# Performance work log

Hardware: AMD Instinct MI355X
Metric: run time of the kernel (lower is better)

Reference implementation:

```python
import jax, jax.numpy as jnp
from jax import lax
import numpy as np

BS, L, D, K, R, VOCAB = 4096, 200, 64, 4, 3, 100000
DROP = jnp.float32(-(1 << 31))


def squash(caps):
    # caps: (bs, K, D)
    n = jnp.linalg.norm(caps, axis=2, keepdims=True)   # (bs, K, 1)
    n2 = n * n
    return n2 / ((1.0 + n2) * n + 1e-9) * caps


def setup_inputs() -> dict:
    key = jax.random.key(0)
    ks = jax.random.split(key, 8)
    his = jax.random.randint(ks[0], (BS, L), 0, VOCAB)                     # item ids, 0 = pad
    E = jax.random.normal(ks[1], (VOCAB, D), dtype=jnp.float32)            # itemEmbeds.weight
    S = jax.random.normal(ks[2], (D, D), dtype=jnp.float32)                # bilinear map S
    B0 = jax.random.normal(ks[3], (K, L), dtype=jnp.float32)               # routing logits
    lim1 = 1.0 / np.sqrt(D)
    W1 = jax.random.uniform(ks[4], (D, 4 * D), jnp.float32, -lim1, lim1)   # dense1 (in, out)
    b1 = jax.random.uniform(ks[5], (4 * D,), jnp.float32, -lim1, lim1)
    lim2 = 1.0 / np.sqrt(4 * D)
    W2 = jax.random.uniform(ks[6], (4 * D, D), jnp.float32, -lim2, lim2)   # dense2 (in, out)
    b2 = jax.random.uniform(ks[7], (D,), jnp.float32, -lim2, lim2)
    return {"his": his, "E": E, "S": S, "B0": B0, "W1": W1, "b1": b1, "W2": W2, "b2": b2}


def reference(his, E, S, B0, W1, b1, W2, b2):
    bs = his.shape[0]
    # padding_idx=0 -> embedding row 0 is zero
    E = E.at[0].set(0.0)
    mask = (his != 0)[:, None, :]                       # (bs, 1, L), broadcasts over K
    hisP = jnp.einsum('bld,de->ble', E[his], S)         # (bs, L, D)
    hisPd = lax.stop_gradient(hisP)                     # routing updates run under no_grad
    B = jnp.broadcast_to(lax.stop_gradient(B0)[None], (bs, K, L))
    for _ in range(R - 1):
        W = jax.nn.softmax(jnp.where(mask, B, DROP), axis=2)   # (bs, K, L)
        caps = squash(jnp.einsum('bkl,bld->bkd', W, hisPd))
        B = B + jnp.einsum('bkd,bld->bkl', caps, hisPd)
    W = jax.nn.softmax(jnp.where(mask, B, DROP), axis=2)
    caps = squash(jnp.einsum('bkl,bld->bkd', W, hisP))         # differentiable last iter
    h = jax.nn.relu(jnp.einsum('bkd,df->bkf', caps, W1) + b1)
    return jnp.einsum('bkf,fd->bkd', h, W2) + b2               # (bs, K, D)
```

## Files before the change

kernel.cpp:

```cpp
#include <hip/hip_runtime.h>

#define LSEQ 200
#define KCAP 4
#define NVOC 100000

__global__ __launch_bounds__(256) void precompute_P(
    const float* __restrict__ E, const float* __restrict__ S,
    float* __restrict__ P)
{
    __shared__ __align__(16) float Sl[64 * 64];
    __shared__ __align__(16) float Et[64 * 68];
    const int tid   = threadIdx.x;
    const int vbase = blockIdx.x * 64;

    #pragma unroll
    for (int t = tid; t < 4096; t += 256) Sl[t] = S[t];
    #pragma unroll
    for (int t = tid; t < 4096; t += 256) {
        int r = t >> 6, e = t & 63;
        int v = vbase + r;
        Et[e * 68 + r] = (v < NVOC) ? E[v * 64 + e] : 0.f;
    }
    __syncthreads();

    const int rq = tid >> 4;
    const int cq = tid & 15;
    float a00=0,a01=0,a02=0,a03=0, a10=0,a11=0,a12=0,a13=0;
    float a20=0,a21=0,a22=0,a23=0, a30=0,a31=0,a32=0,a33=0;
    #pragma unroll 8
    for (int e = 0; e < 64; e++) {
        float4 ev = *(const float4*)(Et + e * 68 + rq * 4);
        float4 sv = *(const float4*)(Sl + e * 64 + cq * 4);
        a00 = fmaf(ev.x, sv.x, a00); a01 = fmaf(ev.x, sv.y, a01);
        a02 = fmaf(ev.x, sv.z, a02); a03 = fmaf(ev.x, sv.w, a03);
        a10 = fmaf(ev.y, sv.x, a10); a11 = fmaf(ev.y, sv.y, a11);
        a12 = fmaf(ev.y, sv.z, a12); a13 = fmaf(ev.y, sv.w, a13);
        a20 = fmaf(ev.z, sv.x, a20); a21 = fmaf(ev.z, sv.y, a21);
        a22 = fmaf(ev.z, sv.z, a22); a23 = fmaf(ev.z, sv.w, a23);
        a30 = fmaf(ev.w, sv.x, a30); a31 = fmaf(ev.w, sv.y, a31);
        a32 = fmaf(ev.w, sv.z, a32); a33 = fmaf(ev.w, sv.w, a33);
    }

    const int r0 = vbase + rq * 4;
    float4 o0 = make_float4(a00, a01, a02, a03);
    float4 o1 = make_float4(a10, a11, a12, a13);
    float4 o2 = make_float4(a20, a21, a22, a23);
    float4 o3 = make_float4(a30, a31, a32, a33);
    if (r0 == 0) o0 = make_float4(0.f, 0.f, 0.f, 0.f);
    if (r0 + 0 < NVOC) *(float4*)(P + (r0 + 0) * 64 + cq * 4) = o0;
    if (r0 + 1 < NVOC) *(float4*)(P + (r0 + 1) * 64 + cq * 4) = o1;
    if (r0 + 2 < NVOC) *(float4*)(P + (r0 + 2) * 64 + cq * 4) = o2;
    if (r0 + 3 < NVOC) *(float4*)(P + (r0 + 3) * 64 + cq * 4) = o3;
}

__global__ __launch_bounds__(256)
__attribute__((amdgpu_waves_per_eu(4, 8)))
void mind_row(
    const int*   __restrict__ his, const float* __restrict__ P,
    const float* __restrict__ B0,  const float* __restrict__ W1,
    const float* __restrict__ b1,  const float* __restrict__ W2,
    const float* __restrict__ b2,  float* __restrict__ out)
{
    __shared__ __align__(16) float POOL[4336];
    float* Bm     = POOL;
    float* W4     = POOL + 832;
    float* caps4  = POOL + 1632;
    float* bigneg = POOL + 1888;
    int*   idxs   = (int*)(POOL + 2088);
    float* SC     = POOL + 2288;
    float* part   = SC;
    float* h4     = SC + 1024;

    const int b    = blockIdx.x;
    const int tid  = threadIdx.x;
    const int lane = tid & 63;
    const int wv   = tid >> 6;

    for (int l = tid; l < LSEQ; l += 256) {
        int id = his[b * LSEQ + l];
        idxs[l]   = id;
        bigneg[l] = (id != 0) ? 0.f : -1e30f;
    }
    if (tid < LSEQ) {
        #pragma unroll
        for (int k = 0; k < KCAP; k++) Bm[k * 208 + tid] = B0[k * LSEQ + tid];
    }
    __syncthreads();

    float hp[50];
    #pragma unroll
    for (int i = 0; i < 50; i++) {
        int l = wv * 50 + i;
        hp[i] = P[idxs[l] * 64 + lane];
    }

    for (int r = 0; r < 3; r++) {
        {
            const float* Bk = Bm + wv * 208;
            float x0 = Bk[lane]       + bigneg[lane];
            float x1 = Bk[lane + 64]  + bigneg[lane + 64];
            float x2 = Bk[lane + 128] + bigneg[lane + 128];
            float x3 = (lane < 8) ? (Bk[lane + 192] + bigneg[lane + 192]) : -3.0e38f;
            float m = fmaxf(fmaxf(x0, x1), fmaxf(x2, x3));
            #pragma unroll
            for (int off = 32; off; off >>= 1) m = fmaxf(m, __shfl_xor(m, off, 64));
            float e0 = __expf(x0 - m), e1 = __expf(x1 - m), e2 = __expf(x2 - m);
            float e3 = (lane < 8) ? __expf(x3 - m) : 0.f;
            float ssum = e0 + e1 + e2 + e3;
            #pragma unroll
            for (int off = 32; off; off >>= 1) ssum += __shfl_xor(ssum, off, 64);
            float inv = 1.f / ssum;
            W4[lane * 4 + wv]         = e0 * inv;
            W4[(lane + 64) * 4 + wv]  = e1 * inv;
            W4[(lane + 128) * 4 + wv] = e2 * inv;
            if (lane < 8) W4[(lane + 192) * 4 + wv] = e3 * inv;
        }
        __syncthreads();

        {
            float a0 = 0, a1 = 0, a2 = 0, a3 = 0;
            #pragma unroll
            for (int i = 0; i < 50; i++) {
                int l = wv * 50 + i;
                float4 w = *(const float4*)(W4 + l * 4);
                float  v = hp[i];
                a0 = fmaf(w.x, v, a0);
                a1 = fmaf(w.y, v, a1);
                a2 = fmaf(w.z, v, a2);
                a3 = fmaf(w.w, v, a3);
            }
            part[wv * 256 + lane]       = a0;
            part[wv * 256 + 64 + lane]  = a1;
            part[wv * 256 + 128 + lane] = a2;
            part[wv * 256 + 192 + lane] = a3;
        }
        __syncthreads();

        {
            float c = part[wv * 64 + lane]       + part[256 + wv * 64 + lane]
                    + part[512 + wv * 64 + lane] + part[768 + wv * 64 + lane];
            float n2 = c * c;
            #pragma unroll
            for (int off = 32; off; off >>= 1) n2 += __shfl_xor(n2, off, 64);
            float n  = sqrtf(n2);
            float sc = n2 / ((1.f + n2) * n + 1e-9f);
            c *= sc;
            caps4[lane * 4 + wv] = c;
        }
        __syncthreads();

        if (r < 2) {
            if (tid < LSEQ) {
                const float4* __restrict__ rowp = (const float4*)(P + idxs[tid] * 64);
                float d0 = 0, d1 = 0, d2 = 0, d3 = 0;
                #pragma unroll
                for (int j = 0; j < 16; j++) {
                    float4 v = rowp[j];
                    {
                        float4 c = *(const float4*)(caps4 + (j * 4 + 0) * 4);
                        d0 = fmaf(c.x, v.x, d0); d1 = fmaf(c.y, v.x, d1);
                        d2 = fmaf(c.z, v.x, d2); d3 = fmaf(c.w, v.x, d3);
                    }
                    {
                        float4 c = *(const float4*)(caps4 + (j * 4 + 1) * 4);
                        d0 = fmaf(c.x, v.y, d0); d1 = fmaf(c.y, v.y, d1);
                        d2 = fmaf(c.z, v.y, d2); d3 = fmaf(c.w, v.y, d3);
                    }
                    {
                        float4 c = *(const float4*)(caps4 + (j * 4 + 2) * 4);
                        d0 = fmaf(c.x, v.z, d0); d1 = fmaf(c.y, v.z, d1);
                        d2 = fmaf(c.z, v.z, d2); d3 = fmaf(c.w, v.z, d3);
                    }
                    {
                        float4 c = *(const float4*)(caps4 + (j * 4 + 3) * 4);
                        d0 = fmaf(c.x, v.w, d0); d1 = fmaf(c.y, v.w, d1);
                        d2 = fmaf(c.z, v.w, d2); d3 = fmaf(c.w, v.w, d3);
                    }
                }
                Bm[tid]       += d0;
                Bm[208 + tid] += d1;
                Bm[416 + tid] += d2;
                Bm[624 + tid] += d3;
            }
            __syncthreads();
        }
    }

    {
        const int f = tid;
        float h0 = 0, h1 = 0, h2 = 0, h3 = 0;
        #pragma unroll 8
        for (int d = 0; d < 64; d++) {
            float  w = W1[d * 256 + f];
            float4 c = *(const float4*)(caps4 + d * 4);
            h0 = fmaf(c.x, w, h0);
            h1 = fmaf(c.y, w, h1);
            h2 = fmaf(c.z, w, h2);
            h3 = fmaf(c.w, w, h3);
        }
        float bb = b1[f];
        h0 = fmaxf(h0 + bb, 0.f);
        h1 = fmaxf(h1 + bb, 0.f);
        h2 = fmaxf(h2 + bb, 0.f);
        h3 = fmaxf(h3 + bb, 0.f);
        h4[f * 4 + 0] = h0; h4[f * 4 + 1] = h1;
        h4[f * 4 + 2] = h2; h4[f * 4 + 3] = h3;
    }
    __syncthreads();

    {
        float o0 = 0, o1 = 0, o2 = 0, o3 = 0;
        #pragma unroll 8
        for (int i = 0; i < 64; i++) {
            int f = wv * 64 + i;
            float  w  = W2[f * 64 + lane];
            float4 hv = *(const float4*)(h4 + f * 4);
            o0 = fmaf(hv.x, w, o0);
            o1 = fmaf(hv.y, w, o1);
            o2 = fmaf(hv.z, w, o2);
            o3 = fmaf(hv.w, w, o3);
        }
        part[wv * 256 + lane]       = o0;
        part[wv * 256 + 64 + lane]  = o1;
        part[wv * 256 + 128 + lane] = o2;
        part[wv * 256 + 192 + lane] = o3;
    }
    __syncthreads();
    {
        float o = part[wv * 64 + lane]       + part[256 + wv * 64 + lane]
                + part[512 + wv * 64 + lane] + part[768 + wv * 64 + lane];
        out[b * 256 + tid] = o + b2[lane];
    }
}

extern "C" void kernel_launch(void* const* d_in, const int* in_sizes, int n_in,
                              void* d_out, int out_size, void* d_ws, size_t ws_size,
                              hipStream_t stream) {
    const int*   his = (const int*)  d_in[0];
    const float* E   = (const float*)d_in[1];
    const float* S   = (const float*)d_in[2];
    const float* B0  = (const float*)d_in[3];
    const float* W1  = (const float*)d_in[4];
    const float* b1  = (const float*)d_in[5];
    const float* W2  = (const float*)d_in[6];
    const float* b2  = (const float*)d_in[7];
    float* out = (float*)d_out;
    float* P   = (float*)d_ws;

    precompute_P<<<(NVOC + 63) / 64, 256, 0, stream>>>(E, S, P);
    mind_row<<<4096, 256, 0, stream>>>(his, P, B0, W1, b1, W2, b2, out);
}
```

Before: 221.9 us.

## Assign one capsule per wave and regather embedding rows instead of register caching

Drops the 50-element per-thread register cache of projected history rows. Each wave now computes one capsule's weighted sum over all 200 positions, reading P rows directly from global memory each round, and the per-wave weights are stored contiguously. This removes the cross-wave partial-sum reduction and two barriers and lowers register pressure, which allows a higher waves-per-EU target. In exchange, every round gathers each row four times from memory through a dependent index load.

New measurement: 314.3 us. 41.6% more time.

```diff
diff --git a/kernel.cpp b/kernel.cpp
--- a/kernel.cpp
+++ b/kernel.cpp
@@ -54,20 +54,20 @@
 }
 
 __global__ __launch_bounds__(256)
-__attribute__((amdgpu_waves_per_eu(4, 8)))
+__attribute__((amdgpu_waves_per_eu(6, 8)))
 void mind_row(
     const int*   __restrict__ his, const float* __restrict__ P,
     const float* __restrict__ B0,  const float* __restrict__ W1,
     const float* __restrict__ b1,  const float* __restrict__ W2,
     const float* __restrict__ b2,  float* __restrict__ out)
 {
-    __shared__ __align__(16) float POOL[4336];
+    __shared__ __align__(16) float POOL[4368];
     float* Bm     = POOL;
-    float* W4     = POOL + 832;
-    float* caps4  = POOL + 1632;
-    float* bigneg = POOL + 1888;
-    int*   idxs   = (int*)(POOL + 2088);
-    float* SC     = POOL + 2288;
+    float* Wk     = POOL + 832;
+    float* caps4  = POOL + 1664;
+    float* bigneg = POOL + 1920;
+    int*   idxs   = (int*)(POOL + 2120);
+    float* SC     = POOL + 2320;
     float* part   = SC;
     float* h4     = SC + 1024;
 
@@ -86,13 +86,6 @@
         for (int k = 0; k < KCAP; k++) Bm[k * 208 + tid] = B0[k * LSEQ + tid];
     }
     __syncthreads();
-
-    float hp[50];
-    #pragma unroll
-    for (int i = 0; i < 50; i++) {
-        int l = wv * 50 + i;
-        hp[i] = P[idxs[l] * 64 + lane];
-    }
 
     for (int r = 0; r < 3; r++) {
         {
@@ -110,35 +103,22 @@
             #pragma unroll
             for (int off = 32; off; off >>= 1) ssum += __shfl_xor(ssum, off, 64);
             float inv = 1.f / ssum;
-            W4[lane * 4 + wv]         = e0 * inv;
-            W4[(lane + 64) * 4 + wv]  = e1 * inv;
-            W4[(lane + 128) * 4 + wv] = e2 * inv;
-            if (lane < 8) W4[(lane + 192) * 4 + wv] = e3 * inv;
-        }
-        __syncthreads();
+            float* Wr = Wk + wv * 208;
+            Wr[lane]       = e0 * inv;
+            Wr[lane + 64]  = e1 * inv;
+            Wr[lane + 128] = e2 * inv;
+            if (lane < 8) Wr[lane + 192] = e3 * inv;
+        }
 
         {
-            float a0 = 0, a1 = 0, a2 = 0, a3 = 0;
-            #pragma unroll
-            for (int i = 0; i < 50; i++) {
-                int l = wv * 50 + i;
-                float4 w = *(const float4*)(W4 + l * 4);
-                float  v = hp[i];
-                a0 = fmaf(w.x, v, a0);
-                a1 = fmaf(w.y, v, a1);
-                a2 = fmaf(w.z, v, a2);
-                a3 = fmaf(w.w, v, a3);
+            const float* Wr = Wk + wv * 208;
+            float c = 0.f;
+            #pragma unroll 8
+            for (int l = 0; l < LSEQ; l++) {
+                float w = Wr[l];
+                float v = P[idxs[l] * 64 + lane];
+                c = fmaf(w, v, c);
             }
-            part[wv * 256 + lane]       = a0;
-            part[wv * 256 + 64 + lane]  = a1;
-            part[wv * 256 + 128 + lane] = a2;
-            part[wv * 256 + 192 + lane] = a3;
-        }
-        __syncthreads();
-
-        {
-            float c = part[wv * 64 + lane]       + part[256 + wv * 64 + lane]
-                    + part[512 + wv * 64 + lane] + part[768 + wv * 64 + lane];
             float n2 = c * c;
             #pragma unroll
             for (int off = 32; off; off >>= 1) n2 += __shfl_xor(n2, off, 64);
```
